# Kernel optimization log

Hardware: AMD Instinct MI355X
Metric: run time of the kernel (lower is better)

The kernel has to match this reference:

```python
import jax, jax.numpy as jnp
import numpy as np

N = 8192        # points
M = 131072      # query-key pairs (edges)
C_IN = 512
H = 8           # heads
D = 64          # head_channels
BINS = 48
BIN_SIZE = 0.05


def setup_inputs() -> dict:
    key = jax.random.key(0)
    ks = jax.random.split(key, 8)
    x_F = jax.random.normal(ks[0], (N, C_IN), dtype=jnp.float32)
    x_C = jax.random.uniform(ks[1], (N, 3), dtype=jnp.float32)
    qk_pair_idxs = jax.random.randint(ks[2], (2, M), 0, N, dtype=jnp.int64)
    W_qkv = jax.random.normal(ks[3], (C_IN, 3 * H * D), dtype=jnp.float32) * 0.02
    b_qkv = jnp.zeros((3 * H * D,), dtype=jnp.float32)
    q_tables = jax.random.normal(ks[4], (3, BINS, H, D), dtype=jnp.float32) * 0.02
    k_tables = jax.random.normal(ks[5], (3, BINS, H, D), dtype=jnp.float32) * 0.02
    v_tables = jax.random.normal(ks[6], (3, BINS, H, D), dtype=jnp.float32) * 0.02
    return {"x_F": x_F, "x_C": x_C, "qk_pair_idxs": qk_pair_idxs,
            "W_qkv": W_qkv, "b_qkv": b_qkv,
            "q_tables": q_tables, "k_tables": k_tables, "v_tables": v_tables}


def reference(x_F, x_C, qk_pair_idxs, W_qkv, b_qkv, q_tables, k_tables, v_tables):
    n = x_F.shape[0]
    qkv = (x_F @ W_qkv + b_qkv).reshape(n, 3, H, D)
    q = qkv[:, 0] * (D ** -0.5)   # scale folded into queries, as in the module
    k = qkv[:, 1]
    v = qkv[:, 2]
    qi = qk_pair_idxs[0]
    ki = qk_pair_idxs[1]
    # quantized relative coordinates -> table bin indices [M,3]
    rel = (x_C[qi] - x_C[ki]) / BIN_SIZE + BINS / 2
    idx = jnp.clip(rel.astype(jnp.int32), 0, BINS - 1)
    # precompute per-point, per-axis, per-bin table dot products [N,3,BINS,H]
    q_dot = jnp.einsum('nhd,abhd->nabh', q, q_tables)
    k_dot = jnp.einsum('nhd,abhd->nabh', k, k_tables)
    # content logits [M,H]
    logits = jnp.einsum('mhd,mhd->mh', q[qi], k[ki])
    for a in range(3):  # fixed xyz axes
        logits = logits + q_dot[qi, a, idx[:, a]] + k_dot[ki, a, idx[:, a]]
    # scatter softmax over query index (per head)
    seg_max = jax.ops.segment_max(logits, qi, num_segments=n)
    e = jnp.exp(logits - seg_max[qi])
    denom = jax.ops.segment_sum(e, qi, num_segments=n)
    attn = e / denom[qi]  # [M,H]
    # value-side relative position bias, summed over axes [M,H,D]
    vt = v_tables[0, idx[:, 0]] + v_tables[1, idx[:, 1]] + v_tables[2, idx[:, 2]]
    contrib = attn[:, :, None] * (v[ki] + vt)            # [M,H,D]
    agg = jax.ops.segment_sum(contrib, qi, num_segments=n)  # [N,H,D]
    return agg.reshape(n, H * D)
```

## Files before the change

kernel.cpp:

```cpp
#include <hip/hip_runtime.h>
#include <hip/hip_bf16.h>
#include <stdint.h>

#define N_PTS 8192
#define M_EDGES 131072
#define CIN 512
#define QKV_COLS 1536

typedef __bf16 bf16x8 __attribute__((ext_vector_type(8)));
typedef float f32x4 __attribute__((ext_vector_type(4)));

#define GAS __attribute__((address_space(1)))
#define LAS __attribute__((address_space(3)))

__device__ __forceinline__ void gload_lds16(const void* g, void* l) {
  __builtin_amdgcn_global_load_lds((const GAS void*)g, (LAS void*)l, 16, 0, 0);
}

__global__ __launch_bounds__(256) void prep_kernel(
    const float* __restrict__ xF, const float* __restrict__ W,
    const float* __restrict__ qt, const float* __restrict__ kt,
    const float* __restrict__ vt, const int* __restrict__ pairs,
    const float* __restrict__ xc,
    __bf16* __restrict__ A, __bf16* __restrict__ BT,
    __bf16* __restrict__ qtb, __bf16* __restrict__ ktb, __bf16* __restrict__ vtT,
    int* __restrict__ qi_a, unsigned* __restrict__ pack0, int* __restrict__ cnt) {
  __shared__ float tile[32][33];
  int b = blockIdx.x;
  int tid = threadIdx.x;
  if (b < 4096) {
    int base = (b * 256 + tid) * 4;
    float4 v = *(const float4*)(xF + base);
    A[base + 0] = (__bf16)v.x;
    A[base + 1] = (__bf16)v.y;
    A[base + 2] = (__bf16)v.z;
    A[base + 3] = (__bf16)v.w;
  } else if (b < 4864) {
    int blk = b - 4096;
    int bk = blk & 15, bn = blk >> 4;
    int x = tid & 31, y = tid >> 5;
#pragma unroll
    for (int j = 0; j < 4; j++) {
      int r = y + j * 8;
      tile[r][x] = W[(size_t)(bk * 32 + r) * QKV_COLS + bn * 32 + x];
    }
    __syncthreads();
#pragma unroll
    for (int j = 0; j < 4; j++) {
      int r = y + j * 8;
      BT[(size_t)(bn * 32 + r) * CIN + bk * 32 + x] = (__bf16)tile[x][r];
    }
  } else if (b < 5152) {
    int i = (b - 4864) * 256 + tid;
    int d = i & 63, h = (i >> 6) & 7, ab = i >> 9;
    int po = (h * 144 + ab) * 64 + d;
    qtb[po] = (__bf16)qt[i];
    ktb[po] = (__bf16)kt[i];
  } else if (b < 5472) {
    int i = (b - 5152) * 256 + tid;
    int p = i % 160;
    int d = (i / 160) & 63;
    int h = i / 10240;
    vtT[i] = (p < 144) ? (__bf16)vt[p * 512 + h * 64 + d] : (__bf16)0.f;
  } else {
    int m = (b - 5472) * 256 + tid;
    int qi = pairs[m], ki = pairs[M_EDGES + m];
    unsigned pb = 0;
#pragma unroll
    for (int a = 0; a < 3; a++) {
      float rel = (xc[qi * 3 + a] - xc[ki * 3 + a]) / 0.05f + 24.0f;
      int bb = (int)rel;
      bb = bb < 0 ? 0 : (bb > 47 ? 47 : bb);
      pb |= (unsigned)bb << (6 * a);
    }
    qi_a[m] = qi;
    pack0[m] = (unsigned)ki | (pb << 13);
    atomicAdd(&cnt[qi], 1);
  }
}

__global__ __launch_bounds__(256) void gemm_scan_kernel(
    const __bf16* __restrict__ A, const __bf16* __restrict__ BT,
    const float* __restrict__ bias, __bf16* __restrict__ qb,
    __bf16* __restrict__ kv,
    const int* __restrict__ cnt, int* __restrict__ off, int* __restrict__ cursor,
    int* __restrict__ qperm) {
  __shared__ __align__(16) char At[128 * 128];
  __shared__ __align__(16) char Bt[128 * 128];
  __shared__ int wsum[4];
  __shared__ int hist2[64];
  __shared__ int bpos[64];
  int bid = blockIdx.x;
  int tid = threadIdx.x;

  if (bid == 768) {
    int lane = tid & 63, w = tid >> 6;
    int local[32];
    int s = 0;
#pragma unroll
    for (int i = 0; i < 8; i++) {
      int4 v = ((const int4*)cnt)[tid * 8 + i];
      local[i * 4 + 0] = v.x; local[i * 4 + 1] = v.y;
      local[i * 4 + 2] = v.z; local[i * 4 + 3] = v.w;
      s += v.x + v.y + v.z + v.w;
    }
    int incl = s;
#pragma unroll
    for (int d = 1; d < 64; d <<= 1) {
      int t = __shfl_up(incl, d, 64);
      if (lane >= d) incl += t;
    }
    if (lane == 63) wsum[w] = incl;
    if (tid < 64) hist2[tid] = 0;
    __syncthreads();
    int woff = 0;
#pragma unroll
    for (int j = 0; j < 4; j++) woff += (j < w) ? wsum[j] : 0;
    int run = woff + incl - s;
    int base = tid * 32;
#pragma unroll
    for (int i = 0; i < 32; i++) {
      off[base + i] = run;
      cursor[base + i] = run;
      run += local[i];
      int c = local[i] < 63 ? local[i] : 63;
      atomicAdd(&hist2[c], 1);
    }
    if (tid == 255) off[N_PTS] = run;
    __syncthreads();
    if (tid < 64) {
      int p = 0;
      for (int bb = 63; bb > tid; bb--) p += hist2[bb];
      bpos[tid] = p;
    }
    __syncthreads();
#pragma unroll
    for (int i = 0; i < 32; i++) {
      int c = local[i] < 63 ? local[i] : 63;
      int pos = atomicAdd(&bpos[c], 1);
      qperm[pos] = base + i;
    }
    return;
  }

  int bn = bid % 12, bm = bid / 12;
  int w = tid >> 6, l = tid & 63;
  int wm = w & 1, wn = w >> 1;
  f32x4 acc[4][4] = {};
  const char* Ab = (const char*)A;
  const char* Bb = (const char*)BT;
  int lr = l & 15;
  int lk = (l >> 4) * 16;
  int xr = (lr & 7) << 4;

  for (int kt = 0; kt < 8; kt++) {
#pragma unroll
    for (int r = 0; r < 4; r++) {
      int flat = r * 4096 + tid * 16;
      int row = flat >> 7, colb = flat & 127;
      int gcolb = colb ^ ((row & 7) << 4);
      gload_lds16(Ab + ((size_t)(bm * 128 + row) * CIN + kt * 64) * 2 + gcolb,
                  At + r * 4096 + w * 1024);
      gload_lds16(Bb + ((size_t)(bn * 128 + row) * CIN + kt * 64) * 2 + gcolb,
                  Bt + r * 4096 + w * 1024);
    }
    __syncthreads();
#pragma unroll
    for (int ks = 0; ks < 2; ks++) {
      bf16x8 af[4], bfr[4];
      int cs = (ks * 64 + lk) ^ xr;
#pragma unroll
      for (int mf = 0; mf < 4; mf++) af[mf] = *(const bf16x8*)(At + (wm * 64 + mf * 16 + lr) * 128 + cs);
#pragma unroll
      for (int nf = 0; nf < 4; nf++) bfr[nf] = *(const bf16x8*)(Bt + (wn * 64 + nf * 16 + lr) * 128 + cs);
#pragma unroll
      for (int mf = 0; mf < 4; mf++)
#pragma unroll
        for (int nf = 0; nf < 4; nf++)
          acc[mf][nf] = __builtin_amdgcn_mfma_f32_16x16x32_bf16(af[mf], bfr[nf], acc[mf][nf], 0, 0, 0);
    }
    __syncthreads();
  }

  int lg = l >> 4;
#pragma unroll
  for (int mf = 0; mf < 4; mf++) {
#pragma unroll
    for (int nf = 0; nf < 4; nf++) {
      int gc = bn * 128 + wn * 64 + nf * 16 + lr;
      float b = bias[gc];
      int which = gc >> 9;
      int col = gc & 511;
      float scale = which == 0 ? 0.125f : 1.0f;
#pragma unroll
      for (int j = 0; j < 4; j++) {
        int gr = bm * 128 + wm * 64 + mf * 16 + lg * 4 + j;
        float val = (acc[mf][nf][j] + b) * scale;
        if (which == 0) qb[(size_t)gr * 512 + col] = (__bf16)val;
        else kv[(size_t)gr * 1024 + (which == 2 ? 512 : 0) + col] = (__bf16)val;
      }
    }
  }
}

__global__ __launch_bounds__(256) void td_scatter_kernel(
    const __bf16* __restrict__ qb, const __bf16* __restrict__ kv,
    const __bf16* __restrict__ qtb, const __bf16* __restrict__ ktb,
    __bf16* __restrict__ qdot, __bf16* __restrict__ kdot,
    const int* __restrict__ qi_a, const unsigned* __restrict__ pack0,
    int* __restrict__ cursor, unsigned* __restrict__ epack) {
  __shared__ __align__(16) char As[128 * 128];
  __shared__ __align__(16) char Bs[144 * 128];
  int bid = blockIdx.x;
  int tid = threadIdx.x;

  if (bid < 512) {
    int m = bid * 256 + tid;
    int qi = qi_a[m];
    int pos = atomicAdd(&cursor[qi], 1);
    epack[pos] = pack0[m];
    return;
  }

  int td = bid - 512;
  int nt = td & 63, h = (td >> 6) & 7, z = td >> 9;
  const __bf16* src = z ? kv : qb;
  const __bf16* tab = z ? ktb : qtb;
  __bf16* out = z ? kdot : qdot;
  size_t SB = z ? 2048 : 1024;
  int w = tid >> 6, l = tid & 63;
  const char* sb = (const char*)src;
  const char* tb = (const char*)tab + (size_t)h * 144 * 128;
#pragma unroll
  for (int p = 0; p < 4; p++) {
    int flat = p * 4096 + tid * 16;
    int row = flat >> 7, colb = flat & 127;
    int gcolb = colb ^ ((row & 7) << 4);
    gload_lds16(sb + (size_t)(nt * 128 + row) * SB + h * 128 + gcolb, As + p * 4096 + w * 1024);
    gload_lds16(tb + row * 128 + gcolb, Bs + p * 4096 + w * 1024);
  }
  if (w < 2) {
    int flat = 16384 + w * 1024 + l * 16;
    int row = flat >> 7, colb = flat & 127;
    int gcolb = colb ^ ((row & 7) << 4);
    gload_lds16(tb + row * 128 + gcolb, Bs + 16384 + w * 1024);
  }
  __syncthreads();

  f32x4 acc[2][9] = {};
  int lr = l & 15, lk = (l >> 4) * 16;
  int xr = (lr & 7) << 4;
#pragma unroll
  for (int ks = 0; ks < 2; ks++) {
    bf16x8 af[2], bf[9];
    int cs = (ks * 64 + lk) ^ xr;
#pragma unroll
    for (int mf = 0; mf < 2; mf++)
      af[mf] = *(const bf16x8*)(As + (w * 32 + mf * 16 + lr) * 128 + cs);
#pragma unroll
    for (int nf = 0; nf < 9; nf++)
      bf[nf] = *(const bf16x8*)(Bs + (nf * 16 + lr) * 128 + cs);
#pragma unroll
    for (int mf = 0; mf < 2; mf++)
#pragma unroll
      for (int nf = 0; nf < 9; nf++)
        acc[mf][nf] = __builtin_amdgcn_mfma_f32_16x16x32_bf16(af[mf], bf[nf], acc[mf][nf], 0, 0, 0);
  }

  int lg = l >> 4;
#pragma unroll
  for (int mf = 0; mf < 2; mf++)
#pragma unroll
    for (int nf = 0; nf < 9; nf++)
#pragma unroll
      for (int j = 0; j < 4; j++) {
        int n = nt * 128 + w * 32 + mf * 16 + lg * 4 + j;
        int ab = nf * 16 + lr;
        out[(size_t)n * 1152 + ab * 8 + h] = (__bf16)acc[mf][nf][j];
      }
}

__global__ __launch_bounds__(256) void attn_kernel(
    const __bf16* __restrict__ qb, const __bf16* __restrict__ kv,
    const __bf16* __restrict__ qdot, const __bf16* __restrict__ kdot,
    const int* __restrict__ off, const unsigned* __restrict__ epack,
    const int* __restrict__ qperm,
    __bf16* __restrict__ numb, float* __restrict__ den, __bf16* __restrict__ Hb) {
  __shared__ float hist[8 * 164];
  __shared__ float part[4][512];
  __shared__ float dpart[4][8];
  int n = qperm[blockIdx.x];
  int tid = threadIdx.x;
  int w = tid >> 6, l = tid & 63;
  int h = l >> 3, dg = l & 7;

  for (int i = tid; i < 8 * 164; i += 256) hist[i] = 0.f;
  __syncthreads();

  bf16x8 q8 = *(const bf16x8*)(qb + (n << 9) + l * 8);
  float qv[8];
#pragma unroll
  for (int j = 0; j < 8; j++) qv[j] = (float)q8[j];

  float acc[8] = {0.f, 0.f, 0.f, 0.f, 0.f, 0.f, 0.f, 0.f};
  float dn = 0.f;
  int e0 = off[n], e1 = off[n + 1];
  const __bf16* qd_row = qdot + (size_t)n * 1152;
  int axis = dg < 3 ? dg : dg - 3;
  int tsh = 6 * axis;

  int e = e0 + w;
  unsigned pk_next = (e < e1) ? epack[__builtin_amdgcn_readfirstlane(e)] : 0u;
  for (; e < e1; e += 4) {
    unsigned pk = pk_next;
    int en = e + 4;
    if (en < e1) pk_next = epack[__builtin_amdgcn_readfirstlane(en)];
    int ki = pk & 8191;
    unsigned pb = pk >> 13;
    bf16x8 k8 = *(const bf16x8*)(kv + ((size_t)ki << 10) + l * 8);
    bf16x8 v8 = *(const bf16x8*)(kv + ((size_t)ki << 10) + 512 + l * 8);
    int bin = (int)((pb >> tsh) & 63u);
    int idx = (axis * 48 + bin) * 8 + h;
    const __bf16* tbl = dg < 3 ? qd_row : (kdot + (size_t)ki * 1152);
    float p = (dg < 6) ? (float)tbl[idx] : 0.f;
#pragma unroll
    for (int j = 0; j < 8; j++) p += qv[j] * (float)k8[j];
    p += __shfl_xor(p, 1, 64);
    p += __shfl_xor(p, 2, 64);
    p += __shfl_xor(p, 4, 64);
    float x = __expf(p);
    dn += x;
#pragma unroll
    for (int j = 0; j < 8; j++) acc[j] += x * (float)v8[j];
    if (dg < 3) {
      atomicAdd(hist + h * 164 + dg * 48 + (int)((pb >> (6 * dg)) & 63u), x);
    }
  }

  f32x4 a0 = {acc[0], acc[1], acc[2], acc[3]};
  f32x4 a1 = {acc[4], acc[5], acc[6], acc[7]};
  *(f32x4*)&part[w][l * 8] = a0;
  *(f32x4*)&part[w][l * 8 + 4] = a1;
  if (dg == 0) dpart[w][h] = dn;
  __syncthreads();

#pragma unroll
  for (int half = 0; half < 2; half++) {
    int idx = tid + half * 256;
    float s = part[0][idx] + part[1][idx] + part[2][idx] + part[3][idx];
    numb[(n << 9) + idx] = (__bf16)s;
  }
  if (tid < 8) {
    den[n * 8 + tid] = dpart[0][tid] + dpart[1][tid] + dpart[2][tid] + dpart[3][tid];
  }
  if (tid < 160) {
    int row = tid / 20, p = (tid % 20) * 8;
    const float* hp = hist + row * 164 + p;
    bf16x8 o;
#pragma unroll
    for (int j = 0; j < 8; j++) o[j] = (__bf16)hp[j];
    *(bf16x8*)(Hb + (size_t)n * 1280 + row * 160 + p) = o;
  }
}

__global__ __launch_bounds__(256) void finish_kernel(const __bf16* __restrict__ Hb,
                                                     const __bf16* __restrict__ vtT,
                                                     const __bf16* __restrict__ numb,
                                                     const float* __restrict__ den,
                                                     float* __restrict__ out) {
  __shared__ __align__(16) char As[2][128 * 64];
  __shared__ __align__(16) char Bs[2][64 * 64];
  int nt = blockIdx.x, h = blockIdx.y;
  int tid = threadIdx.x, w = tid >> 6, l = tid & 63;
  int lr = l & 15, lk = (l >> 4) * 16;
  int xr = (lr & 3) << 4;
  const char* Ab = (const char*)Hb;
  const char* Bb = (const char*)vtT;
  f32x4 acc[2][4] = {};

  auto stage = [&](int tk, int buf) {
#pragma unroll
    for (int c = 0; c < 2; c++) {
      int flat = c * 4096 + tid * 16;
      int row = flat >> 6, colb = flat & 63;
      int gcolb = colb ^ ((row & 3) << 4);
      gload_lds16(Ab + ((size_t)(nt * 128 + row) * 1280 + h * 160 + tk * 32) * 2 + gcolb,
                  As[buf] + c * 4096 + w * 1024);
    }
    {
      int flat = tid * 16;
      int row = flat >> 6, colb = flat & 63;
      int gcolb = colb ^ ((row & 3) << 4);
      gload_lds16(Bb + ((size_t)(h * 64 + row) * 160 + tk * 32) * 2 + gcolb,
                  Bs[buf] + w * 1024);
    }
  };

  stage(0, 0);
  __syncthreads();
  int cur = 0;
  for (int kt = 0; kt < 5; kt++) {
    if (kt < 4) stage(kt + 1, cur ^ 1);
    bf16x8 af[2], bf[4];
    int cs = lk ^ xr;
#pragma unroll
    for (int mf = 0; mf < 2; mf++) af[mf] = *(const bf16x8*)(As[cur] + (w * 32 + mf * 16 + lr) * 64 + cs);
#pragma unroll
    for (int nf = 0; nf < 4; nf++) bf[nf] = *(const bf16x8*)(Bs[cur] + (nf * 16 + lr) * 64 + cs);
#pragma unroll
    for (int mf = 0; mf < 2; mf++)
#pragma unroll
      for (int nf = 0; nf < 4; nf++)
        acc[mf][nf] = __builtin_amdgcn_mfma_f32_16x16x32_bf16(af[mf], bf[nf], acc[mf][nf], 0, 0, 0);
    __syncthreads();
    cur ^= 1;
  }

  int lg = l >> 4;
#pragma unroll
  for (int mf = 0; mf < 2; mf++) {
#pragma unroll
    for (int j = 0; j < 4; j++) {
      int n = nt * 128 + w * 32 + mf * 16 + lg * 4 + j;
      float dnv = den[n * 8 + h];
      float inv = dnv > 0.f ? 1.f / dnv : 0.f;
#pragma unroll
      for (int nf = 0; nf < 4; nf++) {
        int gi = (n << 9) + h * 64 + nf * 16 + lr;
        out[gi] = ((float)numb[gi] + acc[mf][nf][j]) * inv;
      }
    }
  }
}

extern "C" void kernel_launch(void* const* d_in, const int* in_sizes, int n_in,
                              void* d_out, int out_size, void* d_ws, size_t ws_size,
                              hipStream_t stream) {
  const float* xF = (const float*)d_in[0];
  const float* xC = (const float*)d_in[1];
  const int* pairs = (const int*)d_in[2];
  const float* W = (const float*)d_in[3];
  const float* bias = (const float*)d_in[4];
  const float* qt = (const float*)d_in[5];
  const float* kt = (const float*)d_in[6];
  const float* vt = (const float*)d_in[7];
  float* out = (float*)d_out;

  char* ws = (char*)d_ws;
  size_t o = 0;
  auto alloc = [&](size_t bytes) {
    void* p = ws + o;
    o = (o + bytes + 255) & ~(size_t)255;
    return p;
  };
  char* region0 = (char*)alloc((size_t)N_PTS * 1280 * 2);
  __bf16* A = (__bf16*)region0;
  __bf16* BT = (__bf16*)(region0 + (size_t)N_PTS * CIN * 2);
  __bf16* Hb = (__bf16*)region0;
  __bf16* qb = (__bf16*)alloc((size_t)N_PTS * 512 * 2);
  __bf16* kv = (__bf16*)alloc((size_t)N_PTS * 1024 * 2);
  __bf16* qtb = (__bf16*)alloc((size_t)8 * 144 * 64 * 2);
  __bf16* ktb = (__bf16*)alloc((size_t)8 * 144 * 64 * 2);
  __bf16* vtT = (__bf16*)alloc((size_t)8 * 64 * 160 * 2);
  __bf16* qdot = (__bf16*)alloc((size_t)N_PTS * 1152 * 2);
  __bf16* kdot = (__bf16*)alloc((size_t)N_PTS * 1152 * 2);
  __bf16* numb = (__bf16*)alloc((size_t)N_PTS * 512 * 2);
  float* den = (float*)alloc((size_t)N_PTS * 8 * 4);
  int* qi_a = (int*)alloc(M_EDGES * 4);
  unsigned* pack0 = (unsigned*)alloc(M_EDGES * 4);
  unsigned* epack = (unsigned*)alloc(M_EDGES * 4);
  int* cnt = (int*)alloc(N_PTS * 4);
  int* off = (int*)alloc((N_PTS + 1) * 4);
  int* cursor = (int*)alloc(N_PTS * 4);
  int* qperm = (int*)alloc(N_PTS * 4);

  hipMemsetAsync(cnt, 0, N_PTS * 4, stream);

  prep_kernel<<<5984, 256, 0, stream>>>(xF, W, qt, kt, vt, pairs, xC,
                                        A, BT, qtb, ktb, vtT, qi_a, pack0, cnt);
  gemm_scan_kernel<<<769, 256, 0, stream>>>(A, BT, bias, qb, kv, cnt, off, cursor, qperm);
  td_scatter_kernel<<<1536, 256, 0, stream>>>(qb, kv, qtb, ktb, qdot, kdot,
                                              qi_a, pack0, cursor, epack);
  attn_kernel<<<N_PTS, 256, 0, stream>>>(qb, kv, qdot, kdot, off, epack, qperm,
                                         numb, den, Hb);
  finish_kernel<<<dim3(N_PTS / 128, 8), 256, 0, stream>>>(Hb, vtT, numb, den, out);
}
```

Baseline: 142.7 us.

## Fuse value-table bias matmul into attention kernel with sparse bin list

Removes the separate finish GEMM kernel. Each attention block now builds a compact list of the table bins its edges actually touch, then adds the weighted value-table rows and normalizes straight into the output. This avoids writing and re-reading the per-point histogram, numerator and denominator buffers, and it drops one launch and the transposed padded value-table prep. The cost is a serial per-block loop over the occupied bins, which reads the bf16 value table from global memory instead of using MFMA.

```diff
diff --git a/kernel.cpp b/kernel.cpp
--- a/kernel.cpp
+++ b/kernel.cpp
@@ -23,7 +23,7 @@
     const float* __restrict__ vt, const int* __restrict__ pairs,
     const float* __restrict__ xc,
     __bf16* __restrict__ A, __bf16* __restrict__ BT,
-    __bf16* __restrict__ qtb, __bf16* __restrict__ ktb, __bf16* __restrict__ vtT,
+    __bf16* __restrict__ qtb, __bf16* __restrict__ ktb, __bf16* __restrict__ vtb,
     int* __restrict__ qi_a, unsigned* __restrict__ pack0, int* __restrict__ cnt) {
   __shared__ float tile[32][33];
   int b = blockIdx.x;
@@ -56,14 +56,9 @@
     int po = (h * 144 + ab) * 64 + d;
     qtb[po] = (__bf16)qt[i];
     ktb[po] = (__bf16)kt[i];
-  } else if (b < 5472) {
-    int i = (b - 5152) * 256 + tid;
-    int p = i % 160;
-    int d = (i / 160) & 63;
-    int h = i / 10240;
-    vtT[i] = (p < 144) ? (__bf16)vt[p * 512 + h * 64 + d] : (__bf16)0.f;
+    vtb[i] = (__bf16)vt[i];
   } else {
-    int m = (b - 5472) * 256 + tid;
+    int m = (b - 5152) * 256 + tid;
     int qi = pairs[m], ki = pairs[M_EDGES + m];
     unsigned pb = 0;
 #pragma unroll
@@ -283,18 +278,22 @@
 __global__ __launch_bounds__(256) void attn_kernel(
     const __bf16* __restrict__ qb, const __bf16* __restrict__ kv,
     const __bf16* __restrict__ qdot, const __bf16* __restrict__ kdot,
-    const int* __restrict__ off, const unsigned* __restrict__ epack,
-    const int* __restrict__ qperm,
-    __bf16* __restrict__ numb, float* __restrict__ den, __bf16* __restrict__ Hb) {
+    const __bf16* __restrict__ vtb, const int* __restrict__ off,
+    const unsigned* __restrict__ epack, const int* __restrict__ qperm,
+    float* __restrict__ out) {
   __shared__ float hist[8 * 164];
   __shared__ float part[4][512];
   __shared__ float dpart[4][8];
+  __shared__ float den_s[8];
+  __shared__ short binlist[144];
+  __shared__ int bincnt;
   int n = qperm[blockIdx.x];
   int tid = threadIdx.x;
   int w = tid >> 6, l = tid & 63;
   int h = l >> 3, dg = l & 7;
 
   for (int i = tid; i < 8 * 164; i += 256) hist[i] = 0.f;
+  if (tid == 0) bincnt = 0;
   __syncthreads();
 
   bf16x8 q8 = *(const bf16x8*)(qb + (n << 9) + l * 8);
@@ -344,93 +343,30 @@
   if (dg == 0) dpart[w][h] = dn;
   __syncthreads();
 
-#pragma unroll
-  for (int half = 0; half < 2; half++) {
-    int idx = tid + half * 256;
-    float s = part[0][idx] + part[1][idx] + part[2][idx] + part[3][idx];
-    numb[(n << 9) + idx] = (__bf16)s;
-  }
-  if (tid < 8) {
-    den[n * 8 + tid] = dpart[0][tid] + dpart[1][tid] + dpart[2][tid] + dpart[3][tid];
-  }
-  if (tid < 160) {
-    int row = tid / 20, p = (tid % 20) * 8;
-    const float* hp = hist + row * 164 + p;
-    bf16x8 o;
-#pragma unroll
-    for (int j = 0; j < 8; j++) o[j] = (__bf16)hp[j];
-    *(bf16x8*)(Hb + (size_t)n * 1280 + row * 160 + p) = o;
-  }
-}
-
-__global__ __launch_bounds__(256) void finish_kernel(const __bf16* __restrict__ Hb,
-                                                     const __bf16* __restrict__ vtT,
-                                                     const __bf16* __restrict__ numb,
-                                                     const float* __restrict__ den,
-                                                     float* __restrict__ out) {
-  __shared__ __align__(16) char As[2][128 * 64];
-  __shared__ __align__(16) char Bs[2][64 * 64];
-  int nt = blockIdx.x, h = blockIdx.y;
-  int tid = threadIdx.x, w = tid >> 6, l = tid & 63;
-  int lr = l & 15, lk = (l >> 4) * 16;
-  int xr = (lr & 3) << 4;
-  const char* Ab = (const char*)Hb;
-  const char* Bb = (const char*)vtT;
-  f32x4 acc[2][4] = {};
-
-  auto stage = [&](int tk, int buf) {
-#pragma unroll
-    for (int c = 0; c < 2; c++) {
-      int flat = c * 4096 + tid * 16;
-      int row = flat >> 6, colb = flat & 63;
-      int gcolb = colb ^ ((row & 3) << 4);
-      gload_lds16(Ab + ((size_t)(nt * 128 + row) * 1280 + h * 160 + tk * 32) * 2 + gcolb,
-                  As[buf] + c * 4096 + w * 1024);
-    }
-    {
-      int flat = tid * 16;
-      int row = flat >> 6, colb = flat & 63;
-      int gcolb = colb ^ ((row & 3) << 4);
-      gload_lds16(Bb + ((size_t)(h * 64 + row) * 160 + tk * 32) * 2 + gcolb,
-                  Bs[buf] + w * 1024);
-    }
-  };
-
-  stage(0, 0);
+  if (tid < 8)
+    den_s[tid] = dpart[0][tid] + dpart[1][tid] + dpart[2][tid] + dpart[3][tid];
+  if (tid < 144 && hist[tid] > 0.f) {
+    int pos = atomicAdd(&bincnt, 1);
+    binlist[pos] = (short)tid;
+  }
   __syncthreads();
-  int cur = 0;
-  for (int kt = 0; kt < 5; kt++) {
-    if (kt < 4) stage(kt + 1, cur ^ 1);
-    bf16x8 af[2], bf[4];
-    int cs = lk ^ xr;
-#pragma unroll
-    for (int mf = 0; mf < 2; mf++) af[mf] = *(const bf16x8*)(As[cur] + (w * 32 + mf * 16 + lr) * 64 + cs);
-#pragma unroll
-    for (int nf = 0; nf < 4; nf++) bf[nf] = *(const bf16x8*)(Bs[cur] + (nf * 16 + lr) * 64 + cs);
-#pragma unroll
-    for (int mf = 0; mf < 2; mf++)
-#pragma unroll
-      for (int nf = 0; nf < 4; nf++)
-        acc[mf][nf] = __builtin_amdgcn_mfma_f32_16x16x32_bf16(af[mf], bf[nf], acc[mf][nf], 0, 0, 0);
-    __syncthreads();
-    cur ^= 1;
-  }
-
-  int lg = l >> 4;
-#pragma unroll
-  for (int mf = 0; mf < 2; mf++) {
-#pragma unroll
-    for (int j = 0; j < 4; j++) {
-      int n = nt * 128 + w * 32 + mf * 16 + lg * 4 + j;
-      float dnv = den[n * 8 + h];
-      float inv = dnv > 0.f ? 1.f / dnv : 0.f;
-#pragma unroll
-      for (int nf = 0; nf < 4; nf++) {
-        int gi = (n << 9) + h * 64 + nf * 16 + lr;
-        out[gi] = ((float)numb[gi] + acc[mf][nf][j]) * inv;
-      }
-    }
-  }
+
+  int K = bincnt;
+  int idx2 = tid + 256;
+  float s1 = part[0][tid] + part[1][tid] + part[2][tid] + part[3][tid];
+  float s2 = part[0][idx2] + part[1][idx2] + part[2][idx2] + part[3][idx2];
+  int h1 = tid >> 6, h2 = h1 + 4;
+  for (int k = 0; k < K; k++) {
+    int bin = binlist[k];
+    float hv1 = hist[h1 * 164 + bin];
+    float hv2 = hist[h2 * 164 + bin];
+    s1 += hv1 * (float)vtb[bin * 512 + tid];
+    s2 += hv2 * (float)vtb[bin * 512 + idx2];
+  }
+  float i1 = den_s[h1] > 0.f ? 1.f / den_s[h1] : 0.f;
+  float i2 = den_s[h2] > 0.f ? 1.f / den_s[h2] : 0.f;
+  out[(n << 9) + tid] = s1 * i1;
+  out[(n << 9) + idx2] = s2 * i2;
 }
 
 extern "C" void kernel_launch(void* const* d_in, const int* in_sizes, int n_in,
@@ -453,19 +389,15 @@
     o = (o + bytes + 255) & ~(size_t)255;
     return p;
   };
-  char* region0 = (char*)alloc((size_t)N_PTS * 1280 * 2);
-  __bf16* A = (__bf16*)region0;
-  __bf16* BT = (__bf16*)(region0 + (size_t)N_PTS * CIN * 2);
-  __bf16* Hb = (__bf16*)region0;
+  __bf16* A = (__bf16*)alloc((size_t)N_PTS * CIN * 2);
+  __bf16* BT = (__bf16*)alloc((size_t)QKV_COLS * CIN * 2);
   __bf16* qb = (__bf16*)alloc((size_t)N_PTS * 512 * 2);
   __bf16* kv = (__bf16*)alloc((size_t)N_PTS * 1024 * 2);
   __bf16* qtb = (__bf16*)alloc((size_t)8 * 144 * 64 * 2);
   __bf16* ktb = (__bf16*)alloc((size_t)8 * 144 * 64 * 2);
-  __bf16* vtT = (__bf16*)alloc((size_t)8 * 64 * 160 * 2);
+  __bf16* vtb = (__bf16*)alloc((size_t)144 * 512 * 2);
   __bf16* qdot = (__bf16*)alloc((size_t)N_PTS * 1152 * 2);
   __bf16* kdot = (__bf16*)alloc((size_t)N_PTS * 1152 * 2);
-  __bf16* numb = (__bf16*)alloc((size_t)N_PTS * 512 * 2);
-  float* den = (float*)alloc((size_t)N_PTS * 8 * 4);
   int* qi_a = (int*)alloc(M_EDGES * 4);
   unsigned* pack0 = (unsigned*)alloc(M_EDGES * 4);
   unsigned* epack = (unsigned*)alloc(M_EDGES * 4);
@@ -476,12 +408,10 @@
 
   hipMemsetAsync(cnt, 0, N_PTS * 4, stream);
 
-  prep_kernel<<<5984, 256, 0, stream>>>(xF, W, qt, kt, vt, pairs, xC,
-                                        A, BT, qtb, ktb, vtT, qi_a, pack0, cnt);
+  prep_kernel<<<5664, 256, 0, stream>>>(xF, W, qt, kt, vt, pairs, xC,
+                                        A, BT, qtb, ktb, vtb, qi_a, pack0, cnt);
   gemm_scan_kernel<<<769, 256, 0, stream>>>(A, BT, bias, qb, kv, cnt, off, cursor, qperm);
   td_scatter_kernel<<<1536, 256, 0, stream>>>(qb, kv, qtb, ktb, qdot, kdot,
                                               qi_a, pack0, cursor, epack);
-  attn_kernel<<<N_PTS, 256, 0, stream>>>(qb, kv, qdot, kdot, off, epack, qperm,
-                                         numb, den, Hb);
-  finish_kernel<<<dim3(N_PTS / 128, 8), 256, 0, stream>>>(Hb, vtT, numb, den, out);
-}
+  attn_kernel<<<N_PTS, 256, 0, stream>>>(qb, kv, qdot, kdot, vtb, off, epack, qperm, out);
+}
```

New measurement: 146.4 us. 2.6% more time.
